# Optimization experiments

Hardware: AMD Instinct MI355X
Metric: run time of the kernel (lower is better)

## Reference

```python
import jax, jax.numpy as jnp
import numpy as np

NODES = [2048, 4096, 8192]
LAMB = 0.5  # sparsity penalty, applied only at layer 0


def tanh_deriv(x):
    t = jnp.tanh(x)
    return 1.0 - t * t


def setup_inputs() -> dict:
    key = jax.random.key(0)
    k1, k2, k3, k4 = jax.random.split(key, 4)
    B = 256
    batch_inp = jax.random.normal(k1, (B, NODES[2]), jnp.float32)
    # torch Linear weight layout: (out_features, in_features)
    W0 = jax.random.normal(k2, (NODES[1], NODES[0]), jnp.float32) / np.float32(np.sqrt(NODES[0]))
    W1 = jax.random.normal(k3, (NODES[2], NODES[1]), jnp.float32) / np.float32(np.sqrt(NODES[1]))
    memory = jax.random.normal(k4, (NODES[0],), jnp.float32) * 0.1
    return {"batch_inp": batch_inp, "W0": W0, "W1": W1, "memory": memory,
            "n_iters": 8, "inf_lr": 0.05}


def reference(batch_inp, W0, W1, memory, n_iters, inf_lr):
    B = batch_inp.shape[0]
    inf_lr = jnp.float32(inf_lr)

    def compute_errs(v0, v1, v2):
        # update_err_nodes: e_l = v_l - pred_l
        e0 = v0 - memory
        e1 = v1 - jnp.tanh(v0) @ W0.T   # [B, n1]
        e2 = v2 - jnp.tanh(v1) @ W1.T   # [B, n2]
        return e0, e1, e2

    def energy(e0, e1, e2):
        return (jnp.sum(e0 * e0) + jnp.sum(e1 * e1) + jnp.sum(e2 * e2)) * (100.0 / B)

    # set_nodes: v0 = memory (broadcast over batch -- identical to torch broadcasting),
    # v1 = forward prediction, v2 clamped to input.
    v0 = jnp.broadcast_to(memory, (B, NODES[0]))
    v1 = jnp.tanh(v0) @ W0.T
    v2 = batch_inp
    e0, e1, e2 = compute_errs(v0, v1, v2)

    def step(carry, _):
        v0, v1, e0, e1, e2 = carry
        # update_val_nodes (torch.no_grad block): all errs are pre-update values
        d0 = -e0 - LAMB * jnp.sign(v0) + tanh_deriv(v0) * (e1 @ W0)
        nv0 = jax.lax.stop_gradient(jax.nn.relu(v0 + inf_lr * d0))
        d1 = -e1 + tanh_deriv(v1) * (e2 @ W1)
        nv1 = jax.lax.stop_gradient(jax.nn.relu(v1 + inf_lr * d1))
        ne0, ne1, ne2 = compute_errs(nv0, nv1, v2)
        return (nv0, nv1, ne0, ne1, ne2), energy(ne0, ne1, ne2)

    _, losses = jax.lax.scan(step, (v0, v1, e0, e1, e2), None, length=n_iters)
    return losses  # [n_iters] per-iteration energies (inf_losses)
```

## Files before the change

### kernel.cpp

```cpp
#include <hip/hip_runtime.h>
#include <hip/hip_bf16.h>
#include <stdint.h>


typedef short short8x __attribute__((ext_vector_type(8)));
typedef float float4x __attribute__((ext_vector_type(4)));
typedef unsigned short u16;
typedef u16 u16x8 __attribute__((ext_vector_type(8)));

static constexpr float LOSS_SCALE = 100.0f / 256.0f;

__device__ __forceinline__ u16 f2b(float x) {
    union { float f; uint32_t u; } v{x};
    uint32_t b = v.u + 0x7fffu + ((v.u >> 16) & 1u);
    return (u16)(b >> 16);
}

__device__ __forceinline__ float signf_(float x) {
    return (x > 0.f) ? 1.f : ((x < 0.f) ? -1.f : 0.f);
}

__device__ __forceinline__ void gload_lds16(const void* g, void* lds) {
    __builtin_amdgcn_global_load_lds(
        (const __attribute__((address_space(1))) void*)g,
        (__attribute__((address_space(3))) void*)lds, 16, 0, 0);
}

__global__ void k_zero(float* p, int n) {
    int i = blockIdx.x * blockDim.x + threadIdx.x;
    if (i < n) p[i] = 0.f;
}

__global__ __launch_bounds__(256) void k_cast_both(
    const float* __restrict__ in, u16* __restrict__ outN, u16* __restrict__ outT,
    int R, int C) {
    __shared__ float tile[32][33];
    int x = blockIdx.x * 32 + threadIdx.x;
#pragma unroll
    for (int k = 0; k < 32; k += 8) {
        int y = blockIdx.y * 32 + threadIdx.y + k;
        float v = in[(size_t)y * C + x];
        tile[threadIdx.y + k][threadIdx.x] = v;
        outN[(size_t)y * C + x] = f2b(v);
    }
    __syncthreads();
    int ox = blockIdx.y * 32 + threadIdx.x;
#pragma unroll
    for (int k = 0; k < 32; k += 8) {
        int oy = blockIdx.x * 32 + threadIdx.y + k;
        outT[(size_t)oy * R + ox] = f2b(tile[threadIdx.x][threadIdx.y + k]);
    }
}

__global__ void k_fill_v0(float* __restrict__ v0, const float* __restrict__ memory,
                          int n, int mask) {
    int i = blockIdx.x * blockDim.x + threadIdx.x;
    if (i < n) v0[i] = memory[i & mask];
}

__global__ void k_tanh(float* __restrict__ dst, const float* __restrict__ src, int n) {
    int i = blockIdx.x * blockDim.x + threadIdx.x;
    if (i < n) dst[i] = tanhf(src[i]);
}

__global__ void k_rowdot(const float* __restrict__ x, const float* __restrict__ W,
                         float* __restrict__ out, int K) {
    int i = blockIdx.x;
    const float* w = W + (size_t)i * K;
    float s = 0.f;
    for (int j = threadIdx.x; j < K; j += 256) s += x[j] * w[j];
    __shared__ float red[256];
    red[threadIdx.x] = s;
    __syncthreads();
    for (int st = 128; st > 0; st >>= 1) {
        if (threadIdx.x < st) red[threadIdx.x] += red[threadIdx.x + st];
        __syncthreads();
    }
    if (threadIdx.x == 0) out[i] = red[0];
}

__global__ void k_bcast_v1_e1(float* __restrict__ v1, float* __restrict__ e1,
                              u16* __restrict__ e1b,
                              const float* __restrict__ r1, int n, int mask) {
    int i = blockIdx.x * blockDim.x + threadIdx.x;
    if (i < n) { v1[i] = r1[i & mask]; e1[i] = 0.f; e1b[i] = 0; }
}

__global__ void k_e2_init(u16* __restrict__ e2b, const float* __restrict__ inp,
                          const float* __restrict__ r2, int n, int mask) {
    int i = blockIdx.x * blockDim.x + threadIdx.x;
    if (i < n) e2b[i] = f2b(inp[i] - r2[i & mask]);
}

struct GDR {
    const u16* A;
    const u16* Bt;
    const float* x0;
    const float* x1;
    float* y0;
    u16* y0b;
    u16* y1b;
    float* loss;
    const float* lr;
    int N, K, nCol;
};

template <int EPI>
__device__ void gemm_tile(const GDR& g, int tile, u16* stage, float* red8) {
    const int t = threadIdx.x;
    const int w = t >> 6, l = t & 63;
    const int lm = l & 15, lq = l >> 4;
    const int rowBlk = tile / g.nCol, colBlk = tile - rowBlk * g.nCol;
    const int row0 = rowBlk * 64, col0 = colBlk * 64;
    const int K = g.K;
    const int Ksl = K >> 3;
    const int nCh = Ksl >> 5;

    u16* base = stage + (w << 13);
    const u16* aSrc = g.A + (size_t)(row0 + (l >> 2)) * K + w * Ksl + (l & 3) * 8;
    const u16* bSrc = g.Bt + (size_t)(col0 + (l >> 2)) * K + w * Ksl + (l & 3) * 8;
    const size_t rStep = (size_t)16 * K;

    int aoff[4], boff[4];
#pragma unroll
    for (int i = 0; i < 4; ++i) { aoff[i] = (i * 16 + lm) * 32 + lq * 8; boff[i] = aoff[i]; }

    float4x acc[4][4];
#pragma unroll
    for (int i = 0; i < 4; ++i)
#pragma unroll
        for (int j = 0; j < 4; ++j) acc[i][j] = (float4x)0.f;

#define ISSUE(c, b) { \
    u16* ab = base + (b) * 4096; \
    const u16* as = aSrc + (c) * 32; \
    const u16* bs = bSrc + (c) * 32; \
    gload_lds16(as, ab);             gload_lds16(as + rStep, ab + 512); \
    gload_lds16(as + 2*rStep, ab + 1024); gload_lds16(as + 3*rStep, ab + 1536); \
    gload_lds16(bs, ab + 2048);      gload_lds16(bs + rStep, ab + 2560); \
    gload_lds16(bs + 2*rStep, ab + 3072); gload_lds16(bs + 3*rStep, ab + 3584); }

#define COMPUTE(b) { \
    u16* ab = base + (b) * 4096; \
    short8x a[4], bb[4]; \
    _Pragma("unroll") for (int i = 0; i < 4; ++i) a[i] = *(const short8x*)(ab + aoff[i]); \
    _Pragma("unroll") for (int j = 0; j < 4; ++j) bb[j] = *(const short8x*)(ab + 2048 + boff[j]); \
    _Pragma("unroll") for (int i = 0; i < 4; ++i) \
    _Pragma("unroll") for (int j = 0; j < 4; ++j) \
        acc[i][j] = __builtin_amdgcn_mfma_f32_16x16x32_bf16(a[i], bb[j], acc[i][j], 0, 0, 0); }

    ISSUE(0, 0);
    int c = 0;
    for (; c < nCh - 1; ++c) {
        __builtin_amdgcn_sched_barrier(0);
        ISSUE(c + 1, (c + 1) & 1);
        __builtin_amdgcn_sched_barrier(0);
        __builtin_amdgcn_s_waitcnt(0x0F78);
        __builtin_amdgcn_sched_barrier(0);
        COMPUTE(c & 1);
    }
    __builtin_amdgcn_sched_barrier(0);
    __builtin_amdgcn_s_waitcnt(0x0F70);
    __builtin_amdgcn_sched_barrier(0);
    COMPUTE(c & 1);
#undef ISSUE
#undef COMPUTE

    float* T = (float*)stage;
    __syncthreads();
    if (w < 4) {
        float* tw = T + w * 4096;
#pragma unroll
        for (int i = 0; i < 4; ++i)
#pragma unroll
            for (int j = 0; j < 4; ++j)
#pragma unroll
                for (int r = 0; r < 4; ++r)
                    tw[(i * 16 + lq * 4 + r) * 64 + j * 16 + lm] = acc[i][j][r];
    }
    __syncthreads();
    if (w >= 4) {
        float* tw = T + (w - 4) * 4096;
#pragma unroll
        for (int i = 0; i < 4; ++i)
#pragma unroll
            for (int j = 0; j < 4; ++j)
#pragma unroll
                for (int r = 0; r < 4; ++r)
                    tw[(i * 16 + lq * 4 + r) * 64 + j * 16 + lm] += acc[i][j][r];
    }
    __syncthreads();
    if (w < 2) {
        float* d = T + w * 4096;
        const float* s = T + (w + 2) * 4096;
#pragma unroll
        for (int q = 0; q < 16; ++q) {
            int o = l * 64 + q * 4;
            *(float4x*)(d + o) += *(const float4x*)(s + o);
        }
    }
    __syncthreads();
    if (w < 2) {
        float* d = T + w * 2048;
        const float* s = T + 4096 + w * 2048;
#pragma unroll
        for (int q = 0; q < 8; ++q) {
            int o = l * 32 + q * 4;
            *(float4x*)(d + o) += *(const float4x*)(s + o);
        }
    }
    __syncthreads();

    const int row = t >> 3, c8 = (t & 7) * 8;
    const size_t idx = (size_t)(row0 + row) * g.N + col0 + c8;
    float4x cv[2];
    cv[0] = *(const float4x*)(T + row * 64 + c8);
    cv[1] = *(const float4x*)(T + row * 64 + c8 + 4);

    float lr = 0.f;
    if (EPI == 1 || EPI == 2) lr = *g.lr;
    float lsum = 0.f;

    if (EPI == 1) {
        float4x vv[2], mm[2], nv[2]; u16x8 tb;
        vv[0] = *(const float4x*)(g.x0 + idx);       vv[1] = *(const float4x*)(g.x0 + idx + 4);
        mm[0] = *(const float4x*)(g.x1 + col0 + c8); mm[1] = *(const float4x*)(g.x1 + col0 + c8 + 4);
#pragma unroll
        for (int h = 0; h < 2; ++h)
#pragma unroll
            for (int e = 0; e < 4; ++e) {
                float v = vv[h][e], th = tanhf(v), td = 1.f - th * th;
                float d0 = (mm[h][e] - v) - 0.5f * signf_(v) + td * cv[h][e];
                float x = v + lr * d0;
                x = x > 0.f ? x : 0.f;
                nv[h][e] = x;
                tb[h * 4 + e] = f2b(tanhf(x));
                float ne0 = x - mm[h][e];
                lsum += ne0 * ne0;
            }
        *(float4x*)(g.y0 + idx) = nv[0];
        *(float4x*)(g.y0 + idx + 4) = nv[1];
        *(u16x8*)(g.y1b + idx) = tb;
    } else if (EPI == 2) {
        float4x vv[2], ee[2], nv[2]; u16x8 tb;
        vv[0] = *(const float4x*)(g.x0 + idx);     vv[1] = *(const float4x*)(g.x0 + idx + 4);
        ee[0] = *(const float4x*)(g.x1 + idx);     ee[1] = *(const float4x*)(g.x1 + idx + 4);
#pragma unroll
        for (int h = 0; h < 2; ++h)
#pragma unroll
            for (int e = 0; e < 4; ++e) {
                float v = vv[h][e], th = tanhf(v), td = 1.f - th * th;
                float x = v + lr * (-ee[h][e] + td * cv[h][e]);
                x = x > 0.f ? x : 0.f;
                nv[h][e] = x;
                tb[h * 4 + e] = f2b(tanhf(x));
            }
        *(float4x*)(g.y0 + idx) = nv[0];
        *(float4x*)(g.y0 + idx + 4) = nv[1];
        *(u16x8*)(g.y1b + idx) = tb;
    } else if (EPI == 3) {
        float4x vv[2], ne[2]; u16x8 nb;
        vv[0] = *(const float4x*)(g.x0 + idx);     vv[1] = *(const float4x*)(g.x0 + idx + 4);
#pragma unroll
        for (int h = 0; h < 2; ++h)
#pragma unroll
            for (int e = 0; e < 4; ++e) {
                float x = vv[h][e] - cv[h][e];
                ne[h][e] = x;
                nb[h * 4 + e] = f2b(x);
                lsum += x * x;
            }
        *(float4x*)(g.y0 + idx) = ne[0];
        *(float4x*)(g.y0 + idx + 4) = ne[1];
        *(u16x8*)(g.y0b + idx) = nb;
    } else {
        float4x vv[2]; u16x8 nb;
        vv[0] = *(const float4x*)(g.x0 + idx);     vv[1] = *(const float4x*)(g.x0 + idx + 4);
#pragma unroll
        for (int h = 0; h < 2; ++h)
#pragma unroll
            for (int e = 0; e < 4; ++e) {
                float x = vv[h][e] - cv[h][e];
                nb[h * 4 + e] = f2b(x);
                lsum += x * x;
            }
        *(u16x8*)(g.y1b + idx) = nb;
    }

    if (EPI != 2) {
#pragma unroll
        for (int off = 32; off > 0; off >>= 1) lsum += __shfl_down(lsum, off);
        if (l == 0) red8[w] = lsum;
        __syncthreads();
        if (t == 0) {
            float s = 0.f;
#pragma unroll
            for (int q = 0; q < 8; ++q) s += red8[q];
            atomicAdd(g.loss, s * LOSS_SCALE);
        }
    }
}

template <int EPIA, int EPIB>
__global__ __launch_bounds__(512, 2) void pcn_pair(GDR ga, GDR gb, int nA) {
    __shared__ u16 stage[65536];
    __shared__ float red8[8];
    int bx = blockIdx.x;
    if (bx < nA) gemm_tile<EPIA>(ga, bx, stage, red8);
    else         gemm_tile<EPIB>(gb, bx - nA, stage, red8);
}

extern "C" void kernel_launch(void* const* d_in, const int* in_sizes, int n_in,
                              void* d_out, int out_size, void* d_ws, size_t ws_size,
                              hipStream_t stream)
{
    const float* batch_inp = (const float*)d_in[0];
    const float* W0        = (const float*)d_in[1];
    const float* W1        = (const float*)d_in[2];
    const float* memory    = (const float*)d_in[3];
    const float* lr_ptr    = (const float*)d_in[5];
    float* out = (float*)d_out;

    const int n0 = 2048, n1 = 4096, n2 = 8192, Bn = 256;

    char* ws = (char*)d_ws;
    auto alloc_f = [&](size_t n) { float* p = (float*)ws; ws += n * 4; return p; };
    auto alloc_b = [&](size_t n) { u16* p = (u16*)ws; ws += n * 2; return p; };

    float* v0  = alloc_f((size_t)Bn * n0);
    float* v1  = alloc_f((size_t)Bn * n1);
    float* e1  = alloc_f((size_t)Bn * n1);
    u16*   e1b = alloc_b((size_t)Bn * n1);
    u16*   e2b = alloc_b((size_t)Bn * n2);
    u16*   T0b = alloc_b((size_t)Bn * n0);
    u16*   T1b = alloc_b((size_t)Bn * n1);
    u16*   W0b  = alloc_b((size_t)n1 * n0);
    u16*   W0Tb = alloc_b((size_t)n0 * n1);
    u16*   W1b  = alloc_b((size_t)n2 * n1);
    u16*   W1Tb = alloc_b((size_t)n1 * n2);
    float* tm = alloc_f(n0);
    float* r1 = alloc_f(n1);
    float* t1 = alloc_f(n1);
    float* r2 = alloc_f(n2);

    k_zero<<<1, 32, 0, stream>>>(out, 8);
    k_cast_both<<<dim3(n0 / 32, n1 / 32), dim3(32, 8), 0, stream>>>(W0, W0b, W0Tb, n1, n0);
    k_cast_both<<<dim3(n1 / 32, n2 / 32), dim3(32, 8), 0, stream>>>(W1, W1b, W1Tb, n2, n1);
    k_fill_v0<<<(Bn * n0) / 256, 256, 0, stream>>>(v0, memory, Bn * n0, n0 - 1);
    k_tanh<<<n0 / 256, 256, 0, stream>>>(tm, memory, n0);
    k_rowdot<<<n1, 256, 0, stream>>>(tm, W0, r1, n0);
    k_tanh<<<n1 / 256, 256, 0, stream>>>(t1, r1, n1);
    k_bcast_v1_e1<<<(Bn * n1) / 256, 256, 0, stream>>>(v1, e1, e1b, r1, Bn * n1, n1 - 1);
    k_rowdot<<<n2, 256, 0, stream>>>(t1, W1, r2, n1);
    k_e2_init<<<(Bn * n2) / 256, 256, 0, stream>>>(e2b, batch_inp, r2, Bn * n2, n2 - 1);

    for (int it = 0; it < 8; ++it) {
        float* loss = out + it;

        GDR g2{e2b, W1Tb, v1, e1, v1, nullptr, T1b, nullptr, lr_ptr, n1, n2, n1 / 64};
        GDR g1{e1b, W0Tb, v0, memory, v0, nullptr, T0b, loss, lr_ptr, n0, n1, n0 / 64};
        pcn_pair<2, 1><<<4 * (n1 / 64) + 4 * (n0 / 64), 512, 0, stream>>>(
            g2, g1, 4 * (n1 / 64));

        GDR g4{T1b, W1b, batch_inp, nullptr, nullptr, nullptr, e2b, loss, nullptr, n2, n1, n2 / 64};
        GDR g3{T0b, W0b, v1, nullptr, e1, e1b, nullptr, loss, nullptr, n1, n0, n1 / 64};
        pcn_pair<4, 3><<<4 * (n2 / 64) + 4 * (n1 / 64), 512, 0, stream>>>(
            g4, g3, 4 * (n2 / 64));
    }
}
```

Baseline: 1.424 ms.

## Cover full batch per workgroup with 2-way split-K instead of 8-way

Each workgroup now handles a 64-column tile across all four 64-row batch blocks. Its eight waves split into four row blocks times two K halves, replacing the previous 64x64 tile with an 8-way K split. This reuses the B (weight) tile across the whole batch and cuts the LDS reduction steps from four syncs to two. The grid shrinks fourfold, to roughly 96-192 workgroups, which may underfill the GPU's compute units. The fused epilogue now loops over four row blocks.

```diff
diff --git a/kernel.cpp b/kernel.cpp
--- a/kernel.cpp
+++ b/kernel.cpp
@@ -110,15 +110,15 @@
     const int t = threadIdx.x;
     const int w = t >> 6, l = t & 63;
     const int lm = l & 15, lq = l >> 4;
-    const int rowBlk = tile / g.nCol, colBlk = tile - rowBlk * g.nCol;
-    const int row0 = rowBlk * 64, col0 = colBlk * 64;
+    const int col0 = tile * 64;
     const int K = g.K;
-    const int Ksl = K >> 3;
+    const int rb_ = w >> 1, kh = w & 1;
+    const int Ksl = K >> 1;
     const int nCh = Ksl >> 5;
 
     u16* base = stage + (w << 13);
-    const u16* aSrc = g.A + (size_t)(row0 + (l >> 2)) * K + w * Ksl + (l & 3) * 8;
-    const u16* bSrc = g.Bt + (size_t)(col0 + (l >> 2)) * K + w * Ksl + (l & 3) * 8;
+    const u16* aSrc = g.A + (size_t)(rb_ * 64 + (l >> 2)) * K + kh * Ksl + (l & 3) * 8;
+    const u16* bSrc = g.Bt + (size_t)(col0 + (l >> 2)) * K + kh * Ksl + (l & 3) * 8;
     const size_t rStep = (size_t)16 * K;
 
     int aoff[4], boff[4];
@@ -168,8 +168,8 @@
 
     float* T = (float*)stage;
     __syncthreads();
-    if (w < 4) {
-        float* tw = T + w * 4096;
+    if (kh) {
+        float* tw = T + rb_ * 4096;
 #pragma unroll
         for (int i = 0; i < 4; ++i)
 #pragma unroll
@@ -179,8 +179,8 @@
                     tw[(i * 16 + lq * 4 + r) * 64 + j * 16 + lm] = acc[i][j][r];
     }
     __syncthreads();
-    if (w >= 4) {
-        float* tw = T + (w - 4) * 4096;
+    if (!kh) {
+        float* tw = T + rb_ * 4096;
 #pragma unroll
         for (int i = 0; i < 4; ++i)
 #pragma unroll
@@ -190,101 +190,85 @@
                     tw[(i * 16 + lq * 4 + r) * 64 + j * 16 + lm] += acc[i][j][r];
     }
     __syncthreads();
-    if (w < 2) {
-        float* d = T + w * 4096;
-        const float* s = T + (w + 2) * 4096;
-#pragma unroll
-        for (int q = 0; q < 16; ++q) {
-            int o = l * 64 + q * 4;
-            *(float4x*)(d + o) += *(const float4x*)(s + o);
-        }
-    }
-    __syncthreads();
-    if (w < 2) {
-        float* d = T + w * 2048;
-        const float* s = T + 4096 + w * 2048;
-#pragma unroll
-        for (int q = 0; q < 8; ++q) {
-            int o = l * 32 + q * 4;
-            *(float4x*)(d + o) += *(const float4x*)(s + o);
-        }
-    }
-    __syncthreads();
 
     const int row = t >> 3, c8 = (t & 7) * 8;
-    const size_t idx = (size_t)(row0 + row) * g.N + col0 + c8;
-    float4x cv[2];
-    cv[0] = *(const float4x*)(T + row * 64 + c8);
-    cv[1] = *(const float4x*)(T + row * 64 + c8 + 4);
-
     float lr = 0.f;
     if (EPI == 1 || EPI == 2) lr = *g.lr;
     float lsum = 0.f;
 
-    if (EPI == 1) {
-        float4x vv[2], mm[2], nv[2]; u16x8 tb;
-        vv[0] = *(const float4x*)(g.x0 + idx);       vv[1] = *(const float4x*)(g.x0 + idx + 4);
-        mm[0] = *(const float4x*)(g.x1 + col0 + c8); mm[1] = *(const float4x*)(g.x1 + col0 + c8 + 4);
-#pragma unroll
-        for (int h = 0; h < 2; ++h)
-#pragma unroll
-            for (int e = 0; e < 4; ++e) {
-                float v = vv[h][e], th = tanhf(v), td = 1.f - th * th;
-                float d0 = (mm[h][e] - v) - 0.5f * signf_(v) + td * cv[h][e];
-                float x = v + lr * d0;
-                x = x > 0.f ? x : 0.f;
-                nv[h][e] = x;
-                tb[h * 4 + e] = f2b(tanhf(x));
-                float ne0 = x - mm[h][e];
-                lsum += ne0 * ne0;
-            }
-        *(float4x*)(g.y0 + idx) = nv[0];
-        *(float4x*)(g.y0 + idx + 4) = nv[1];
-        *(u16x8*)(g.y1b + idx) = tb;
-    } else if (EPI == 2) {
-        float4x vv[2], ee[2], nv[2]; u16x8 tb;
-        vv[0] = *(const float4x*)(g.x0 + idx);     vv[1] = *(const float4x*)(g.x0 + idx + 4);
-        ee[0] = *(const float4x*)(g.x1 + idx);     ee[1] = *(const float4x*)(g.x1 + idx + 4);
-#pragma unroll
-        for (int h = 0; h < 2; ++h)
-#pragma unroll
-            for (int e = 0; e < 4; ++e) {
-                float v = vv[h][e], th = tanhf(v), td = 1.f - th * th;
-                float x = v + lr * (-ee[h][e] + td * cv[h][e]);
-                x = x > 0.f ? x : 0.f;
-                nv[h][e] = x;
-                tb[h * 4 + e] = f2b(tanhf(x));
-            }
-        *(float4x*)(g.y0 + idx) = nv[0];
-        *(float4x*)(g.y0 + idx + 4) = nv[1];
-        *(u16x8*)(g.y1b + idx) = tb;
-    } else if (EPI == 3) {
-        float4x vv[2], ne[2]; u16x8 nb;
-        vv[0] = *(const float4x*)(g.x0 + idx);     vv[1] = *(const float4x*)(g.x0 + idx + 4);
-#pragma unroll
-        for (int h = 0; h < 2; ++h)
-#pragma unroll
-            for (int e = 0; e < 4; ++e) {
-                float x = vv[h][e] - cv[h][e];
-                ne[h][e] = x;
-                nb[h * 4 + e] = f2b(x);
-                lsum += x * x;
-            }
-        *(float4x*)(g.y0 + idx) = ne[0];
-        *(float4x*)(g.y0 + idx + 4) = ne[1];
-        *(u16x8*)(g.y0b + idx) = nb;
-    } else {
-        float4x vv[2]; u16x8 nb;
-        vv[0] = *(const float4x*)(g.x0 + idx);     vv[1] = *(const float4x*)(g.x0 + idx + 4);
-#pragma unroll
-        for (int h = 0; h < 2; ++h)
-#pragma unroll
-            for (int e = 0; e < 4; ++e) {
-                float x = vv[h][e] - cv[h][e];
-                nb[h * 4 + e] = f2b(x);
-                lsum += x * x;
-            }
-        *(u16x8*)(g.y1b + idx) = nb;
+#pragma unroll
+    for (int rb = 0; rb < 4; ++rb) {
+        const float* Tb = T + rb * 4096;
+        const size_t idx = (size_t)(rb * 64 + row) * g.N + col0 + c8;
+        float4x cv[2];
+        cv[0] = *(const float4x*)(Tb + row * 64 + c8);
+        cv[1] = *(const float4x*)(Tb + row * 64 + c8 + 4);
+
+        if (EPI == 1) {
+            float4x vv[2], mm[2], nv[2]; u16x8 tb;
+            vv[0] = *(const float4x*)(g.x0 + idx);       vv[1] = *(const float4x*)(g.x0 + idx + 4);
+            mm[0] = *(const float4x*)(g.x1 + col0 + c8); mm[1] = *(const float4x*)(g.x1 + col0 + c8 + 4);
+#pragma unroll
+            for (int h = 0; h < 2; ++h)
+#pragma unroll
+                for (int e = 0; e < 4; ++e) {
+                    float v = vv[h][e], th = tanhf(v), td = 1.f - th * th;
+                    float d0 = (mm[h][e] - v) - 0.5f * signf_(v) + td * cv[h][e];
+                    float x = v + lr * d0;
+                    x = x > 0.f ? x : 0.f;
+                    nv[h][e] = x;
+                    tb[h * 4 + e] = f2b(tanhf(x));
+                    float ne0 = x - mm[h][e];
+                    lsum += ne0 * ne0;
+                }
+            *(float4x*)(g.y0 + idx) = nv[0];
+            *(float4x*)(g.y0 + idx + 4) = nv[1];
+            *(u16x8*)(g.y1b + idx) = tb;
+        } else if (EPI == 2) {
+            float4x vv[2], ee[2], nv[2]; u16x8 tb;
+            vv[0] = *(const float4x*)(g.x0 + idx);     vv[1] = *(const float4x*)(g.x0 + idx + 4);
+            ee[0] = *(const float4x*)(g.x1 + idx);     ee[1] = *(const float4x*)(g.x1 + idx + 4);
+#pragma unroll
+            for (int h = 0; h < 2; ++h)
+#pragma unroll
+                for (int e = 0; e < 4; ++e) {
+                    float v = vv[h][e], th = tanhf(v), td = 1.f - th * th;
+                    float x = v + lr * (-ee[h][e] + td * cv[h][e]);
+                    x = x > 0.f ? x : 0.f;
+                    nv[h][e] = x;
+                    tb[h * 4 + e] = f2b(tanhf(x));
+                }
+            *(float4x*)(g.y0 + idx) = nv[0];
+            *(float4x*)(g.y0 + idx + 4) = nv[1];
+            *(u16x8*)(g.y1b + idx) = tb;
+        } else if (EPI == 3) {
+            float4x vv[2], ne[2]; u16x8 nb;
+            vv[0] = *(const float4x*)(g.x0 + idx);     vv[1] = *(const float4x*)(g.x0 + idx + 4);
+#pragma unroll
+            for (int h = 0; h < 2; ++h)
+#pragma unroll
+                for (int e = 0; e < 4; ++e) {
+                    float x = vv[h][e] - cv[h][e];
+                    ne[h][e] = x;
+                    nb[h * 4 + e] = f2b(x);
+                    lsum += x * x;
+                }
+            *(float4x*)(g.y0 + idx) = ne[0];
+            *(float4x*)(g.y0 + idx + 4) = ne[1];
+            *(u16x8*)(g.y0b + idx) = nb;
+        } else {
+            float4x vv[2]; u16x8 nb;
+            vv[0] = *(const float4x*)(g.x0 + idx);     vv[1] = *(const float4x*)(g.x0 + idx + 4);
+#pragma unroll
+            for (int h = 0; h < 2; ++h)
+#pragma unroll
+                for (int e = 0; e < 4; ++e) {
+                    float x = vv[h][e] - cv[h][e];
+                    nb[h * 4 + e] = f2b(x);
+                    lsum += x * x;
+                }
+            *(u16x8*)(g.y1b + idx) = nb;
+        }
     }
 
     if (EPI != 2) {
@@ -359,12 +343,10 @@
 
         GDR g2{e2b, W1Tb, v1, e1, v1, nullptr, T1b, nullptr, lr_ptr, n1, n2, n1 / 64};
         GDR g1{e1b, W0Tb, v0, memory, v0, nullptr, T0b, loss, lr_ptr, n0, n1, n0 / 64};
-        pcn_pair<2, 1><<<4 * (n1 / 64) + 4 * (n0 / 64), 512, 0, stream>>>(
-            g2, g1, 4 * (n1 / 64));
+        pcn_pair<2, 1><<<(n1 / 64) + (n0 / 64), 512, 0, stream>>>(g2, g1, n1 / 64);
 
         GDR g4{T1b, W1b, batch_inp, nullptr, nullptr, nullptr, e2b, loss, nullptr, n2, n1, n2 / 64};
         GDR g3{T0b, W0b, v1, nullptr, e1, e1b, nullptr, loss, nullptr, n1, n0, n1 / 64};
-        pcn_pair<4, 3><<<4 * (n2 / 64) + 4 * (n1 / 64), 512, 0, stream>>>(
-            g4, g3, 4 * (n2 / 64));
-    }
-}
+        pcn_pair<4, 3><<<(n2 / 64) + (n1 / 64), 512, 0, stream>>>(g4, g3, n2 / 64);
+    }
+}
```

Result: slower. 1.656 ms (+16.3%).

## Load MFMA fragments directly from global into registers, drop LDS staging

Applied to the files above, without the earlier changes.

Replaces the double-buffered global_load_lds staging of A/B tiles with direct per-lane global loads into register fragments, software-pipelined four chunks deep. The LDS stage buffer is halved since it is now only used for the epilogue reduction. This removes LDS write/read traffic and waitcnt barriers, at the cost of more VGPRs (eight fragment arrays) and less-coalesced global loads, where each lane reads 16 bytes from rows strided by K. The loop assumes nCh is a multiple of 4, which is at least 4.

```diff
diff --git a/kernel.cpp b/kernel.cpp
--- a/kernel.cpp
+++ b/kernel.cpp
@@ -18,12 +18,6 @@
 
 __device__ __forceinline__ float signf_(float x) {
     return (x > 0.f) ? 1.f : ((x < 0.f) ? -1.f : 0.f);
-}
-
-__device__ __forceinline__ void gload_lds16(const void* g, void* lds) {
-    __builtin_amdgcn_global_load_lds(
-        (const __attribute__((address_space(1))) void*)g,
-        (__attribute__((address_space(3))) void*)lds, 16, 0, 0);
 }
 
 __global__ void k_zero(float* p, int n) {
@@ -116,14 +110,9 @@
     const int Ksl = K >> 3;
     const int nCh = Ksl >> 5;
 
-    u16* base = stage + (w << 13);
-    const u16* aSrc = g.A + (size_t)(row0 + (l >> 2)) * K + w * Ksl + (l & 3) * 8;
-    const u16* bSrc = g.Bt + (size_t)(col0 + (l >> 2)) * K + w * Ksl + (l & 3) * 8;
-    const size_t rStep = (size_t)16 * K;
-
-    int aoff[4], boff[4];
-#pragma unroll
-    for (int i = 0; i < 4; ++i) { aoff[i] = (i * 16 + lm) * 32 + lq * 8; boff[i] = aoff[i]; }
+    const u16* aP = g.A + (size_t)(row0 + lm) * K + w * Ksl + lq * 8;
+    const u16* bP = g.Bt + (size_t)(col0 + lm) * K + w * Ksl + lq * 8;
+    const size_t fstep = (size_t)16 * K;
 
     float4x acc[4][4];
 #pragma unroll
@@ -131,40 +120,28 @@
 #pragma unroll
         for (int j = 0; j < 4; ++j) acc[i][j] = (float4x)0.f;
 
-#define ISSUE(c, b) { \
-    u16* ab = base + (b) * 4096; \
-    const u16* as = aSrc + (c) * 32; \
-    const u16* bs = bSrc + (c) * 32; \
-    gload_lds16(as, ab);             gload_lds16(as + rStep, ab + 512); \
-    gload_lds16(as + 2*rStep, ab + 1024); gload_lds16(as + 3*rStep, ab + 1536); \
-    gload_lds16(bs, ab + 2048);      gload_lds16(bs + rStep, ab + 2560); \
-    gload_lds16(bs + 2*rStep, ab + 3072); gload_lds16(bs + 3*rStep, ab + 3584); }
-
-#define COMPUTE(b) { \
-    u16* ab = base + (b) * 4096; \
-    short8x a[4], bb[4]; \
-    _Pragma("unroll") for (int i = 0; i < 4; ++i) a[i] = *(const short8x*)(ab + aoff[i]); \
-    _Pragma("unroll") for (int j = 0; j < 4; ++j) bb[j] = *(const short8x*)(ab + 2048 + boff[j]); \
+#define LOADC(A_, B_, c) { \
+    _Pragma("unroll") for (int i = 0; i < 4; ++i) { \
+        A_[i] = *(const short8x*)(aP + (size_t)i * fstep + (size_t)(c) * 32); \
+        B_[i] = *(const short8x*)(bP + (size_t)i * fstep + (size_t)(c) * 32); } }
+
+#define MM(A_, B_) { \
     _Pragma("unroll") for (int i = 0; i < 4; ++i) \
     _Pragma("unroll") for (int j = 0; j < 4; ++j) \
-        acc[i][j] = __builtin_amdgcn_mfma_f32_16x16x32_bf16(a[i], bb[j], acc[i][j], 0, 0, 0); }
-
-    ISSUE(0, 0);
+        acc[i][j] = __builtin_amdgcn_mfma_f32_16x16x32_bf16(A_[i], B_[j], acc[i][j], 0, 0, 0); }
+
+    short8x a0[4], b0[4], a1[4], b1[4], a2[4], b2[4], a3[4], b3[4];
+    LOADC(a0, b0, 0); LOADC(a1, b1, 1); LOADC(a2, b2, 2); LOADC(a3, b3, 3);
     int c = 0;
-    for (; c < nCh - 1; ++c) {
-        __builtin_amdgcn_sched_barrier(0);
-        ISSUE(c + 1, (c + 1) & 1);
-        __builtin_amdgcn_sched_barrier(0);
-        __builtin_amdgcn_s_waitcnt(0x0F78);
-        __builtin_amdgcn_sched_barrier(0);
-        COMPUTE(c & 1);
-    }
-    __builtin_amdgcn_sched_barrier(0);
-    __builtin_amdgcn_s_waitcnt(0x0F70);
-    __builtin_amdgcn_sched_barrier(0);
-    COMPUTE(c & 1);
-#undef ISSUE
-#undef COMPUTE
+    for (; c + 7 < nCh; c += 4) {
+        MM(a0, b0); LOADC(a0, b0, c + 4);
+        MM(a1, b1); LOADC(a1, b1, c + 5);
+        MM(a2, b2); LOADC(a2, b2, c + 6);
+        MM(a3, b3); LOADC(a3, b3, c + 7);
+    }
+    MM(a0, b0); MM(a1, b1); MM(a2, b2); MM(a3, b3);
+#undef LOADC
+#undef MM
 
     float* T = (float*)stage;
     __syncthreads();
@@ -303,7 +280,7 @@
 
 template <int EPIA, int EPIB>
 __global__ __launch_bounds__(512, 2) void pcn_pair(GDR ga, GDR gb, int nA) {
-    __shared__ u16 stage[65536];
+    __shared__ u16 stage[32768];
     __shared__ float red8[8];
     int bx = blockIdx.x;
     if (bx < nA) gemm_tile<EPIA>(ga, bx, stage, red8);
```

Measured after the change: 1.901 ms. 33.5% more time.
